# Performance work log

Measured on AMD Instinct MI355X. Metric: run time of the kernel, lower is better.

## Reference

```python
import jax, jax.numpy as jnp
import numpy as np

N = 100000
E = 1200000
D = 64
EPS = 1e-5  # BatchNorm1d default eps


def setup_inputs() -> dict:
    key = jax.random.key(0)
    ks = jax.random.split(key, 5)
    x = jax.random.normal(ks[0], (N, D), dtype=jnp.float32)
    edge_index = jax.random.randint(ks[1], (2, E), 0, N, dtype=jnp.int32)
    W1 = jax.random.normal(ks[2], (D, D), dtype=jnp.float32) * (1.0 / np.sqrt(D))
    W2 = jax.random.normal(ks[3], (D, D), dtype=jnp.float32) * (1.0 / np.sqrt(D))
    return {
        'x': x,
        'edge_index': edge_index,
        'W1': W1,
        'b1': jnp.zeros((D,), jnp.float32),
        'gamma1': jnp.ones((D,), jnp.float32),
        'beta1': jnp.zeros((D,), jnp.float32),
        'W2': W2,
        'b2': jnp.zeros((D,), jnp.float32),
        'gamma2': jnp.ones((D,), jnp.float32),
        'beta2': jnp.zeros((D,), jnp.float32),
    }


def gcn_conv(x, src, dst, W, b):
    # GCNConv: xw = x @ W; add self-loops; symmetric deg^{-1/2} normalization;
    # scatter-add aggregation over incoming edges; + bias.
    xw = x @ W  # [N, out]
    # degree including self-loop (edge weight 1)
    deg = jnp.zeros((x.shape[0],), x.dtype).at[dst].add(1.0) + 1.0  # [N]
    dinv = jax.lax.rsqrt(deg)
    norm = dinv[src] * dinv[dst]  # [E]
    agg = jnp.zeros_like(xw).at[dst].add(norm[:, None] * xw[src])
    agg = agg + (dinv * dinv)[:, None] * xw  # self-loop term: deg^{-1} * xw
    return agg + b


def batchnorm(x, gamma, beta):
    # training-mode BatchNorm1d over node dimension (biased variance)
    mu = x.mean(axis=0)
    var = x.var(axis=0)
    return gamma * (x - mu) * jax.lax.rsqrt(var + EPS) + beta


def reference(x, edge_index, W1, b1, gamma1, beta1, W2, b2, gamma2, beta2):
    src, dst = edge_index[0], edge_index[1]
    h = gcn_conv(x, src, dst, W1, b1)
    h = jax.nn.leaky_relu(batchnorm(h, gamma1, beta1), 0.01)
    # dropout p=0.0 -> identity
    h = gcn_conv(h, src, dst, W2, b2)
    h = jax.nn.leaky_relu(batchnorm(h, gamma2, beta2), 0.01)
    return h
```

## Files before the change

### kernel.cpp

```cpp
#include <hip/hip_runtime.h>
#include <hip/hip_bf16.h>

#define NN 100000
#define NE 1200000
#define DD 64
#define EPS 1e-5f

#define NB 196
#define GEMM_BLOCKS (NN / 32)
#define HIST_BLOCKS 256
#define PART_BLOCKS 256
#define EPH ((NE + HIST_BLOCKS - 1) / HIST_BLOCKS)
#define EPB ((NE + PART_BLOCKS - 1) / PART_BLOCKS)

template <bool BN>
__device__ __forceinline__ void gemm_tile(const float* __restrict__ X,
                                          const float* __restrict__ W,
                                          __hip_bfloat16* __restrict__ XWh,
                                          const float* __restrict__ stats,
                                          const float* __restrict__ gamma,
                                          const float* __restrict__ beta,
                                          int blk) {
    __shared__ float xs[32][64];
    __shared__ float sc_s[64], sh_s[64];
    int col = threadIdx.x & 63;
    int rg  = threadIdx.x >> 6;
    int row0 = blk * 32;

    if (BN) {
        if (threadIdx.x < 64) {
            const float inv_n = 1.0f / (float)NN;
            float mu  = stats[threadIdx.x] * inv_n;
            float var = stats[64 + threadIdx.x] * inv_n - mu * mu;
            float sc  = gamma[threadIdx.x] * rsqrtf(var + EPS);
            sc_s[threadIdx.x] = sc;
            sh_s[threadIdx.x] = beta[threadIdx.x] - sc * mu;
        }
        __syncthreads();
    }

    float w[64];
#pragma unroll
    for (int k = 0; k < 64; ++k) w[k] = W[k * 64 + col];

    for (int i = threadIdx.x; i < 32 * 16; i += 256) {
        int r = i >> 4, c4 = i & 15;
        float4 v = ((const float4*)(X + (size_t)(row0 + r) * 64))[c4];
        if (BN) {
            float4 s4 = ((const float4*)sc_s)[c4];
            float4 h4 = ((const float4*)sh_s)[c4];
            v.x = s4.x * v.x + h4.x; v.x = fmaxf(v.x, 0.01f * v.x);
            v.y = s4.y * v.y + h4.y; v.y = fmaxf(v.y, 0.01f * v.y);
            v.z = s4.z * v.z + h4.z; v.z = fmaxf(v.z, 0.01f * v.z);
            v.w = s4.w * v.w + h4.w; v.w = fmaxf(v.w, 0.01f * v.w);
        }
        ((float4*)&xs[r][0])[c4] = v;
    }
    __syncthreads();

    float acc[8];
#pragma unroll
    for (int r8 = 0; r8 < 8; ++r8) {
        int r = rg * 8 + r8;
        float a = 0.0f;
#pragma unroll
        for (int k = 0; k < 64; k += 4) {
            float4 xv = *((const float4*)&xs[r][k]);
            a += xv.x * w[k] + xv.y * w[k + 1] + xv.z * w[k + 2] + xv.w * w[k + 3];
        }
        acc[r8] = a;
    }
#pragma unroll
    for (int r8 = 0; r8 < 8; ++r8)
        XWh[(size_t)(row0 + rg * 8 + r8) * 64 + col] = __float2bfloat16(acc[r8]);
}

__global__ __launch_bounds__(256) void k_hist(const int* __restrict__ dst,
                                              int* __restrict__ cnt196) {
    __shared__ int h[NB];
    for (int t = threadIdx.x; t < NB; t += 256) h[t] = 0;
    __syncthreads();
    int s0 = blockIdx.x * EPH;
    int s1 = s0 + EPH; if (s1 > NE) s1 = NE;
    for (int i = s0 + threadIdx.x; i < s1; i += 256)
        atomicAdd(&h[dst[i] >> 9], 1);
    __syncthreads();
    for (int t = threadIdx.x; t < NB; t += 256)
        if (h[t]) atomicAdd(&cnt196[t], h[t]);
}

__global__ __launch_bounds__(256) void k_scanb(const int* __restrict__ cnt196,
                                               int* __restrict__ bo,
                                               int* __restrict__ cur) {
    __shared__ int s[256];
    int t = threadIdx.x;
    int v = (t < NB) ? cnt196[t] : 0;
    s[t] = v;
    __syncthreads();
    for (int o = 1; o < 256; o <<= 1) {
        int u = (t >= o) ? s[t - o] : 0;
        __syncthreads();
        s[t] += u;
        __syncthreads();
    }
    if (t < NB) {
        int ex = s[t] - v;
        bo[t] = ex;
        cur[t] = ex;
    }
    if (t == 0) bo[NB] = NE;
}

__global__ __launch_bounds__(256) void k_pg(const float* __restrict__ X,
                                            const float* __restrict__ W,
                                            __hip_bfloat16* __restrict__ XWh,
                                            const int* __restrict__ src,
                                            const int* __restrict__ dst,
                                            int* __restrict__ cur,
                                            int* __restrict__ ebuf) {
    if (blockIdx.x < PART_BLOCKS) {
        __shared__ int h[NB];
        for (int t = threadIdx.x; t < NB; t += 256) h[t] = 0;
        __syncthreads();
        int s0 = blockIdx.x * EPB;
        int s1 = s0 + EPB; if (s1 > NE) s1 = NE;
        for (int i = s0 + threadIdx.x; i < s1; i += 256)
            atomicAdd(&h[dst[i] >> 9], 1);
        __syncthreads();
        for (int t = threadIdx.x; t < NB; t += 256) {
            int c = h[t];
            h[t] = c ? atomicAdd(&cur[t], c) : 0;
        }
        __syncthreads();
        for (int i = s0 + threadIdx.x; i < s1; i += 256) {
            int d = dst[i];
            int p = atomicAdd(&h[d >> 9], 1);
            ebuf[p] = src[i] | ((d & 511) << 17);
        }
    } else {
        gemm_tile<false>(X, W, XWh, nullptr, nullptr, nullptr,
                         (int)blockIdx.x - PART_BLOCKS);
    }
}

__global__ __launch_bounds__(256) void k_gemm2(const float* __restrict__ X,
                                               const float* __restrict__ W,
                                               __hip_bfloat16* __restrict__ XWh,
                                               const float* __restrict__ stats,
                                               const float* __restrict__ gamma,
                                               const float* __restrict__ beta) {
    gemm_tile<true>(X, W, XWh, stats, gamma, beta, blockIdx.x);
}

__global__ __launch_bounds__(512) void k_bucket(const int* __restrict__ ebuf,
                                                const int* __restrict__ bo,
                                                int* __restrict__ off,
                                                float* __restrict__ dinv,
                                                int* __restrict__ esrc) {
    __shared__ int s[512];
    int b = blockIdx.x, t = threadIdx.x;
    int base = b << 9;
    int e0 = bo[b], e1 = bo[b + 1];
    s[t] = 0;
    __syncthreads();
    for (int e = e0 + t; e < e1; e += 512)
        atomicAdd(&s[ebuf[e] >> 17], 1);
    __syncthreads();
    int deg = s[t];
    if (base + t < NN) dinv[base + t] = rsqrtf((float)deg + 1.0f);
    for (int o = 1; o < 512; o <<= 1) {
        int u = (t >= o) ? s[t - o] : 0;
        __syncthreads();
        s[t] += u;
        __syncthreads();
    }
    int gstart = e0 + s[t] - deg;
    if (base + t < NN) off[base + t] = gstart;
    if (b == NB - 1 && t == 0) off[NN] = NE;
    __syncthreads();
    s[t] = gstart;
    __syncthreads();
    for (int e = e0 + t; e < e1; e += 512) {
        int v = ebuf[e];
        int p = atomicAdd(&s[v >> 17], 1);
        esrc[p] = v & 0x1FFFF;
    }
}

__device__ __forceinline__ void bf16x8(uint4 u, float* f) {
    f[0] = __uint_as_float(u.x << 16);
    f[1] = __uint_as_float(u.x & 0xFFFF0000u);
    f[2] = __uint_as_float(u.y << 16);
    f[3] = __uint_as_float(u.y & 0xFFFF0000u);
    f[4] = __uint_as_float(u.z << 16);
    f[5] = __uint_as_float(u.z & 0xFFFF0000u);
    f[6] = __uint_as_float(u.w << 16);
    f[7] = __uint_as_float(u.w & 0xFFFF0000u);
}

__global__ __launch_bounds__(256) void k_agg(const __hip_bfloat16* __restrict__ XWh,
                                             const int* __restrict__ off,
                                             const int* __restrict__ esrc,
                                             const float* __restrict__ dinv,
                                             float* __restrict__ out) {
    const uint4* __restrict__ XW4 = (const uint4*)XWh;
    int team = threadIdx.x >> 3;
    int sub  = threadIdx.x & 7;
    int node = blockIdx.x * 32 + team;

    float di = dinv[node];
    float a[8], b[8], c[8], d[8], r0[8], r1[8], r2[8], r3[8];
    uint4 us = XW4[(size_t)node * 8 + sub];
    bf16x8(us, a);
#pragma unroll
    for (int i = 0; i < 8; ++i) { a[i] *= di; b[i] = 0.0f; c[i] = 0.0f; d[i] = 0.0f; }

    int e0 = off[node], e1 = off[node + 1];
    int e = e0;
    for (; e + 3 < e1; e += 4) {
        int s0 = esrc[e];
        int s1 = esrc[e + 1];
        int s2 = esrc[e + 2];
        int s3 = esrc[e + 3];
        float n0 = dinv[s0], n1 = dinv[s1], n2 = dinv[s2], n3 = dinv[s3];
        uint4 u0 = XW4[(size_t)s0 * 8 + sub];
        uint4 u1 = XW4[(size_t)s1 * 8 + sub];
        uint4 u2 = XW4[(size_t)s2 * 8 + sub];
        uint4 u3 = XW4[(size_t)s3 * 8 + sub];
        bf16x8(u0, r0);
        bf16x8(u1, r1);
        bf16x8(u2, r2);
        bf16x8(u3, r3);
#pragma unroll
        for (int i = 0; i < 8; ++i) a[i] += n0 * r0[i];
#pragma unroll
        for (int i = 0; i < 8; ++i) b[i] += n1 * r1[i];
#pragma unroll
        for (int i = 0; i < 8; ++i) c[i] += n2 * r2[i];
#pragma unroll
        for (int i = 0; i < 8; ++i) d[i] += n3 * r3[i];
    }
    for (; e < e1; ++e) {
        int s0 = esrc[e];
        float n0 = dinv[s0];
        uint4 u0 = XW4[(size_t)s0 * 8 + sub];
        bf16x8(u0, r0);
#pragma unroll
        for (int i = 0; i < 8; ++i) a[i] += n0 * r0[i];
    }
#pragma unroll
    for (int i = 0; i < 8; ++i) a[i] = ((a[i] + b[i]) + (c[i] + d[i])) * di;

    float4* o4 = (float4*)out;
    o4[(size_t)node * 16 + sub * 2]     = make_float4(a[0], a[1], a[2], a[3]);
    o4[(size_t)node * 16 + sub * 2 + 1] = make_float4(a[4], a[5], a[6], a[7]);
}

__global__ __launch_bounds__(256) void k_stats(const float* __restrict__ X,
                                               float* __restrict__ stats, int n) {
    __shared__ float ls[4][64], lq[4][64];
    int lane = threadIdx.x & 63, rg = threadIdx.x >> 6;
    float s = 0.0f, sq = 0.0f;
    for (int r = blockIdx.x * 4 + rg; r < n; r += gridDim.x * 4) {
        float v = X[(size_t)r * 64 + lane];
        s += v; sq += v * v;
    }
    ls[rg][lane] = s; lq[rg][lane] = sq;
    __syncthreads();
    if (rg == 0) {
        s  = ls[0][lane] + ls[1][lane] + ls[2][lane] + ls[3][lane];
        sq = lq[0][lane] + lq[1][lane] + lq[2][lane] + lq[3][lane];
        atomicAdd(&stats[lane], s);
        atomicAdd(&stats[64 + lane], sq);
    }
}

__global__ __launch_bounds__(256) void k_bnact(const float* __restrict__ X,
                                               float* __restrict__ Y,
                                               const float* __restrict__ stats,
                                               const float* __restrict__ gamma,
                                               const float* __restrict__ beta,
                                               int n) {
    int lane = threadIdx.x & 63, rg = threadIdx.x >> 6;
    float inv_n = 1.0f / (float)n;
    float mu  = stats[lane] * inv_n;
    float var = stats[64 + lane] * inv_n - mu * mu;
    float sc  = gamma[lane] * rsqrtf(var + EPS);
    float sh  = beta[lane] - sc * mu;
    for (int r = blockIdx.x * 4 + rg; r < n; r += gridDim.x * 4) {
        float v = X[(size_t)r * 64 + lane];
        v = sc * v + sh;
        Y[(size_t)r * 64 + lane] = fmaxf(v, 0.01f * v);
    }
}

extern "C" void kernel_launch(void* const* d_in, const int* in_sizes, int n_in,
                              void* d_out, int out_size, void* d_ws, size_t ws_size,
                              hipStream_t stream) {
    const float* x   = (const float*)d_in[0];
    const int*   ei  = (const int*)d_in[1];
    const int*   src = ei;
    const int*   dst = ei + NE;
    const float* W1  = (const float*)d_in[2];
    const float* g1  = (const float*)d_in[4];
    const float* be1 = (const float*)d_in[5];
    const float* W2  = (const float*)d_in[6];
    const float* g2  = (const float*)d_in[8];
    const float* be2 = (const float*)d_in[9];
    float* out = (float*)d_out;

    char* ws = (char*)d_ws;
    size_t p = 0;
    auto alloc = [&](size_t bytes) {
        size_t o = p;
        p = (p + bytes + 255) & ~(size_t)255;
        return o;
    };
    int*   zeroed  = (int*)(ws + alloc(2048));
    int*   cnt196  = zeroed;
    float* stats   = (float*)(zeroed + 256);
    int*   bo      = (int*)(ws + alloc((size_t)(NB + 1) * 4));
    int*   cur     = (int*)(ws + alloc((size_t)NB * 4));
    int*   ebuf    = (int*)(ws + alloc((size_t)NE * 4));
    int*   esrc    = (int*)(ws + alloc((size_t)NE * 4));
    int*   off     = (int*)(ws + alloc((size_t)(NN + 1) * 4));
    float* dinv    = (float*)(ws + alloc((size_t)NN * 4));
    __hip_bfloat16* Ah = (__hip_bfloat16*)(ws + alloc((size_t)NN * DD * 2));
    float* B       = (float*)(ws + alloc((size_t)NN * DD * 4));
    (void)ws_size; (void)in_sizes; (void)n_in; (void)out_size;

    hipMemsetAsync(zeroed, 0, 2048, stream);

    k_hist<<<HIST_BLOCKS, 256, 0, stream>>>(dst, cnt196);
    k_scanb<<<1, 256, 0, stream>>>(cnt196, bo, cur);
    k_pg<<<PART_BLOCKS + GEMM_BLOCKS, 256, 0, stream>>>(x, W1, Ah, src, dst, cur, ebuf);
    k_bucket<<<NB, 512, 0, stream>>>(ebuf, bo, off, dinv, esrc);

    k_agg<<<NN / 32, 256, 0, stream>>>(Ah, off, esrc, dinv, B);
    k_stats<<<512, 256, 0, stream>>>(B, stats, NN);

    k_gemm2<<<GEMM_BLOCKS, 256, 0, stream>>>(B, W2, Ah, stats, g1, be1);
    k_agg<<<NN / 32, 256, 0, stream>>>(Ah, off, esrc, dinv, B);
    k_stats<<<512, 256, 0, stream>>>(B, stats + 128, NN);
    k_bnact<<<1024, 256, 0, stream>>>(B, out, stats + 128, g2, be2, NN);
}
```

Before: 282.6 us.

## Fuse BN statistics into aggregation and merge histogram with scan

The per-column sum and sum-of-squares for batch norm are now computed inside the aggregation kernel via wavefront shuffles and a shared-memory reduction, followed by atomics. This removes two separate stats kernels that each re-read the full N×64 output. The histogram and bucket scan are also merged into one kernel, with the last-finishing block (detected by an atomic counter) doing the scan, which drops a launch. In exchange, each aggregation block now issues 128 extra atomics and the kernel does more register and shuffle work.

Measured after the change: 357.2 us. +26.4%, slower.

```diff
diff --git a/kernel.cpp b/kernel.cpp
--- a/kernel.cpp
+++ b/kernel.cpp
@@ -75,9 +75,14 @@
         XWh[(size_t)(row0 + rg * 8 + r8) * 64 + col] = __float2bfloat16(acc[r8]);
 }
 
-__global__ __launch_bounds__(256) void k_hist(const int* __restrict__ dst,
-                                              int* __restrict__ cnt196) {
+__global__ __launch_bounds__(256) void k_histscan(const int* __restrict__ dst,
+                                                  int* __restrict__ cnt196,
+                                                  int* __restrict__ done,
+                                                  int* __restrict__ bo,
+                                                  int* __restrict__ cur) {
     __shared__ int h[NB];
+    __shared__ int s[256];
+    __shared__ int lastflag;
     for (int t = threadIdx.x; t < NB; t += 256) h[t] = 0;
     __syncthreads();
     int s0 = blockIdx.x * EPH;
@@ -87,28 +92,28 @@
     __syncthreads();
     for (int t = threadIdx.x; t < NB; t += 256)
         if (h[t]) atomicAdd(&cnt196[t], h[t]);
-}
-
-__global__ __launch_bounds__(256) void k_scanb(const int* __restrict__ cnt196,
-                                               int* __restrict__ bo,
-                                               int* __restrict__ cur) {
-    __shared__ int s[256];
-    int t = threadIdx.x;
-    int v = (t < NB) ? cnt196[t] : 0;
-    s[t] = v;
-    __syncthreads();
-    for (int o = 1; o < 256; o <<= 1) {
-        int u = (t >= o) ? s[t - o] : 0;
-        __syncthreads();
-        s[t] += u;
-        __syncthreads();
-    }
-    if (t < NB) {
-        int ex = s[t] - v;
-        bo[t] = ex;
-        cur[t] = ex;
-    }
-    if (t == 0) bo[NB] = NE;
+    __threadfence();
+    if (threadIdx.x == 0)
+        lastflag = (atomicAdd(done, 1) == HIST_BLOCKS - 1);
+    __syncthreads();
+    if (lastflag) {
+        int t = threadIdx.x;
+        int v = (t < NB) ? atomicAdd(&cnt196[t], 0) : 0;
+        s[t] = v;
+        __syncthreads();
+        for (int o = 1; o < 256; o <<= 1) {
+            int u = (t >= o) ? s[t - o] : 0;
+            __syncthreads();
+            s[t] += u;
+            __syncthreads();
+        }
+        if (t < NB) {
+            int ex = s[t] - v;
+            bo[t] = ex;
+            cur[t] = ex;
+        }
+        if (t == 0) bo[NB] = NE;
+    }
 }
 
 __global__ __launch_bounds__(256) void k_pg(const float* __restrict__ X,
@@ -202,7 +207,9 @@
                                              const int* __restrict__ off,
                                              const int* __restrict__ esrc,
                                              const float* __restrict__ dinv,
-                                             float* __restrict__ out) {
+                                             float* __restrict__ out,
+                                             float* __restrict__ stats) {
+    __shared__ float red[4][128];
     const uint4* __restrict__ XW4 = (const uint4*)XWh;
     int team = threadIdx.x >> 3;
     int sub  = threadIdx.x & 7;
@@ -254,24 +261,30 @@
     float4* o4 = (float4*)out;
     o4[(size_t)node * 16 + sub * 2]     = make_float4(a[0], a[1], a[2], a[3]);
     o4[(size_t)node * 16 + sub * 2 + 1] = make_float4(a[4], a[5], a[6], a[7]);
-}
-
-__global__ __launch_bounds__(256) void k_stats(const float* __restrict__ X,
-                                               float* __restrict__ stats, int n) {
-    __shared__ float ls[4][64], lq[4][64];
-    int lane = threadIdx.x & 63, rg = threadIdx.x >> 6;
-    float s = 0.0f, sq = 0.0f;
-    for (int r = blockIdx.x * 4 + rg; r < n; r += gridDim.x * 4) {
-        float v = X[(size_t)r * 64 + lane];
-        s += v; sq += v * v;
-    }
-    ls[rg][lane] = s; lq[rg][lane] = sq;
-    __syncthreads();
-    if (rg == 0) {
-        s  = ls[0][lane] + ls[1][lane] + ls[2][lane] + ls[3][lane];
-        sq = lq[0][lane] + lq[1][lane] + lq[2][lane] + lq[3][lane];
-        atomicAdd(&stats[lane], s);
-        atomicAdd(&stats[64 + lane], sq);
+
+#pragma unroll
+    for (int i = 0; i < 8; ++i) b[i] = a[i] * a[i];
+#pragma unroll
+    for (int m = 8; m <= 32; m <<= 1) {
+#pragma unroll
+        for (int i = 0; i < 8; ++i) {
+            a[i] += __shfl_xor(a[i], m);
+            b[i] += __shfl_xor(b[i], m);
+        }
+    }
+    int wid = threadIdx.x >> 6;
+    if ((threadIdx.x & 63) < 8) {
+#pragma unroll
+        for (int i = 0; i < 8; ++i) {
+            red[wid][sub * 8 + i]      = a[i];
+            red[wid][64 + sub * 8 + i] = b[i];
+        }
+    }
+    __syncthreads();
+    if (threadIdx.x < 128) {
+        float t = red[0][threadIdx.x] + red[1][threadIdx.x] +
+                  red[2][threadIdx.x] + red[3][threadIdx.x];
+        atomicAdd(&stats[threadIdx.x], t);
     }
 }
 
@@ -316,9 +329,10 @@
         p = (p + bytes + 255) & ~(size_t)255;
         return o;
     };
-    int*   zeroed  = (int*)(ws + alloc(2048));
+    int*   zeroed  = (int*)(ws + alloc(2304));
     int*   cnt196  = zeroed;
     float* stats   = (float*)(zeroed + 256);
+    int*   done    = zeroed + 512;
     int*   bo      = (int*)(ws + alloc((size_t)(NB + 1) * 4));
     int*   cur     = (int*)(ws + alloc((size_t)NB * 4));
     int*   ebuf    = (int*)(ws + alloc((size_t)NE * 4));
@@ -329,18 +343,15 @@
     float* B       = (float*)(ws + alloc((size_t)NN * DD * 4));
     (void)ws_size; (void)in_sizes; (void)n_in; (void)out_size;
 
-    hipMemsetAsync(zeroed, 0, 2048, stream);
-
-    k_hist<<<HIST_BLOCKS, 256, 0, stream>>>(dst, cnt196);
-    k_scanb<<<1, 256, 0, stream>>>(cnt196, bo, cur);
+    hipMemsetAsync(zeroed, 0, 2304, stream);
+
+    k_histscan<<<HIST_BLOCKS, 256, 0, stream>>>(dst, cnt196, done, bo, cur);
     k_pg<<<PART_BLOCKS + GEMM_BLOCKS, 256, 0, stream>>>(x, W1, Ah, src, dst, cur, ebuf);
     k_bucket<<<NB, 512, 0, stream>>>(ebuf, bo, off, dinv, esrc);
 
-    k_agg<<<NN / 32, 256, 0, stream>>>(Ah, off, esrc, dinv, B);
-    k_stats<<<512, 256, 0, stream>>>(B, stats, NN);
+    k_agg<<<NN / 32, 256, 0, stream>>>(Ah, off, esrc, dinv, B, stats);
 
     k_gemm2<<<GEMM_BLOCKS, 256, 0, stream>>>(B, W2, Ah, stats, g1, be1);
-    k_agg<<<NN / 32, 256, 0, stream>>>(Ah, off, esrc, dinv, B);
-    k_stats<<<512, 256, 0, stream>>>(B, stats + 128, NN);
+    k_agg<<<NN / 32, 256, 0, stream>>>(Ah, off, esrc, dinv, B, stats + 128);
     k_bnact<<<1024, 256, 0, stream>>>(B, out, stats + 128, g2, be2, NN);
 }
```
